# Kernel optimization log

Measured on AMD Instinct MI355X. Metric: run time of the kernel, lower is better.

The kernel has to match this reference:

```python
import jax, jax.numpy as jnp
import numpy as np
from jax import lax

DIM = 256
HEADS = 8
EPS = 1e-12  # torch F.normalize default eps
DN = ('NCHW', 'OIHW', 'NCHW')


def conv1x1(x, w):
    return lax.conv_general_dilated(x, w, (1, 1), 'VALID', dimension_numbers=DN)


def dwconv3x3(x, w):
    c = x.shape[1]
    return lax.conv_general_dilated(x, w, (1, 1), ((1, 1), (1, 1)),
                                    dimension_numbers=DN, feature_group_count=c)


def setup_inputs() -> dict:
    key = jax.random.key(0)
    ks = jax.random.split(key, 8)
    B, C, H, W = 4, DIM, 160, 160
    s = lambda fan: 1.0 / np.sqrt(fan)
    return {
        'low': jax.random.normal(ks[0], (B, C, H, W), jnp.float32),
        'high': jax.random.normal(ks[1], (B, C, H, W), jnp.float32),
        'q_w': jax.random.normal(ks[2], (C, C, 1, 1), jnp.float32) * s(C),
        'q_dw_w': jax.random.normal(ks[3], (C, 1, 3, 3), jnp.float32) * s(9),
        'kv_w': jax.random.normal(ks[4], (2 * C, C, 1, 1), jnp.float32) * s(C),
        'kv_dw_w': jax.random.normal(ks[5], (2 * C, 1, 3, 3), jnp.float32) * s(9),
        'proj_w': jax.random.normal(ks[6], (C, C, 1, 1), jnp.float32) * s(C),
        'temperature': jnp.ones((HEADS, 1, 1), jnp.float32),
    }


def reference(low, high, q_w, q_dw_w, kv_w, kv_dw_w, proj_w, temperature):
    B, C, H, W = low.shape
    hw = H * W
    ch = C // HEADS  # channels per head

    q = dwconv3x3(conv1x1(high, q_w), q_dw_w)           # [B, C, H, W]
    kv = dwconv3x3(conv1x1(low, kv_w), kv_dw_w)         # [B, 2C, H, W]
    k, v = jnp.split(kv, 2, axis=1)

    def heads(x):
        return x.reshape(B, HEADS, ch, hw)              # b head c (h w)

    q, k, v = heads(q), heads(k), heads(v)

    # L2-normalize along spatial dim (torch F.normalize semantics)
    q = q / jnp.maximum(jnp.linalg.norm(q, axis=-1, keepdims=True), EPS)
    k = k / jnp.maximum(jnp.linalg.norm(k, axis=-1, keepdims=True), EPS)

    attn = jnp.einsum('bhcn,bhdn->bhcd', q, k) * temperature  # [B, H, ch, ch]
    attn = jax.nn.softmax(attn, axis=-1)
    out = jnp.einsum('bhcd,bhdn->bhcn', attn, v)               # [B, H, ch, hw]

    out = out.reshape(B, C, H, W)
    return conv1x1(out, proj_w)
```

## Files before the change

### kernel.cpp

```cpp
#include <hip/hip_runtime.h>
#include <math.h>

#define HW 25600
#define IMGW 160
#define CDIM 256
#define NB 4
#define NHEADS 8
#define SZB ((long)CDIM * HW)

typedef __attribute__((ext_vector_type(8))) short short8v;
typedef __attribute__((ext_vector_type(4))) float f32x4;
typedef __attribute__((ext_vector_type(8))) unsigned short us8;

union FragU {
    us8 o;
    short8v s;
};

__device__ inline unsigned short f2bf(float f) {
    unsigned u = __float_as_uint(f);
    return (unsigned short)((u + 0x7fffu + ((u >> 16) & 1u)) >> 16);
}
__device__ inline float bf2f(unsigned short h) {
    return __uint_as_float(((unsigned)h) << 16);
}

__global__ __launch_bounds__(256) void cvtw_k(
    const float* __restrict__ w, unsigned short* __restrict__ o,
    int co_off, int nco)
{
    int idx = blockIdx.x * 256 + threadIdx.x;
    if (idx >= nco * 32) return;
    int g2 = idx & 3;
    int kt = (idx >> 2) & 7;
    int co = idx >> 5;
    const float* src = w + (long)(co_off + co) * CDIM + kt * 32 + g2 * 8;
    us8 v;
#pragma unroll
    for (int u = 0; u < 8; ++u) v[u] = f2bf(src[u]);
    int slot = g2 ^ ((co >> 1) & 3);
    *(us8*)(o + ((long)kt * nco + co) * 32 + slot * 8) = v;
}

__global__ __launch_bounds__(256) void cvtT2_k(
    const float* __restrict__ x, unsigned short* __restrict__ xs)
{
    __shared__ float tile[64][65];
    const int t = threadIdx.x;
    const int n0 = blockIdx.x * 64;
    const int c0 = blockIdx.y * 64;
    const long b = blockIdx.z;
    const float* xb = x + b * SZB;
    unsigned short* xo = xs + b * SZB;
#pragma unroll
    for (int it = 0; it < 4; ++it) {
        int row = (t >> 4) + it * 16;
        int col = (t & 15) * 4;
        float4 v = *(const float4*)(xb + (long)(c0 + row) * HW + n0 + col);
        tile[row][col]     = v.x; tile[row][col + 1] = v.y;
        tile[row][col + 2] = v.z; tile[row][col + 3] = v.w;
    }
    __syncthreads();
#pragma unroll
    for (int jt = 0; jt < 2; ++jt) {
        int nl = (t >> 3) + jt * 32;
        int cl = (t & 7) * 8;
        us8 o;
#pragma unroll
        for (int u = 0; u < 8; ++u) o[u] = f2bf(tile[cl + u][nl]);
        int n  = n0 + nl;
        int c  = c0 + cl;
        int kt = c >> 5;
        int g2 = (c >> 3) & 3;
        int slot = g2 ^ ((n >> 1) & 3);
        *(us8*)(xo + ((long)kt * HW + n) * 32 + slot * 8) = o;
    }
}

template<int OUTF32>
__global__ __launch_bounds__(256) void gemm2_k(
    const unsigned short* __restrict__ XS, const unsigned short* __restrict__ WS,
    void* __restrict__ outp, long xbs, long wbs, long obs, int nco)
{
    __shared__ __align__(16) unsigned short Wl[128 * 32];
    __shared__ __align__(16) unsigned short Xl[128 * 32];
    const int t  = threadIdx.x;
    const int l  = t & 63;
    const int wv = t >> 6;
    const int g  = l >> 4;
    const int ln = l & 15;
    const int n0  = blockIdx.x * 128;
    const int co0 = blockIdx.y * 128;
    const long b  = blockIdx.z;
    const unsigned short* Xb = XS + b * xbs;
    const unsigned short* Wb = WS + b * wbs;
    const int wr = wv >> 1, wc = wv & 1;

    f32x4 acc[4][4];
#pragma unroll
    for (int i = 0; i < 4; ++i)
#pragma unroll
        for (int j = 0; j < 4; ++j) acc[i][j] = (f32x4){0.f, 0.f, 0.f, 0.f};

    const int lrow = l >> 2;
    const int lgrp = l & 3;

    for (int kt = 0; kt < 8; ++kt) {
        __syncthreads();
#pragma unroll
        for (int ii = 0; ii < 2; ++ii) {
            int instr = wv * 2 + ii;
            int row = instr * 16 + lrow;
            const unsigned short* wsrc =
                Wb + ((long)kt * nco + co0 + row) * 32 + lgrp * 8;
            __builtin_amdgcn_global_load_lds(
                (const __attribute__((address_space(1))) void*)wsrc,
                (__attribute__((address_space(3))) void*)&Wl[instr * 512], 16, 0, 0);
            const unsigned short* xsrc =
                Xb + ((long)kt * HW + n0 + row) * 32 + lgrp * 8;
            __builtin_amdgcn_global_load_lds(
                (const __attribute__((address_space(1))) void*)xsrc,
                (__attribute__((address_space(3))) void*)&Xl[instr * 512], 16, 0, 0);
        }
        __syncthreads();

        FragU A_[4], B_[4];
#pragma unroll
        for (int i = 0; i < 4; ++i) {
            int row = wr * 64 + i * 16 + ln;
            int slot = g ^ ((row >> 1) & 3);
            A_[i].o = *(const us8*)&Wl[row * 32 + slot * 8];
        }
#pragma unroll
        for (int j = 0; j < 4; ++j) {
            int row = wc * 64 + j * 16 + ln;
            int slot = g ^ ((row >> 1) & 3);
            B_[j].o = *(const us8*)&Xl[row * 32 + slot * 8];
        }
#pragma unroll
        for (int i = 0; i < 4; ++i)
#pragma unroll
            for (int j = 0; j < 4; ++j)
                acc[i][j] = __builtin_amdgcn_mfma_f32_16x16x32_bf16(
                    A_[i].s, B_[j].s, acc[i][j], 0, 0, 0);
    }

    if (OUTF32) {
        float* ob = (float*)outp + b * obs;
#pragma unroll
        for (int i = 0; i < 4; ++i)
#pragma unroll
            for (int j = 0; j < 4; ++j) {
                long ocol = n0 + wc * 64 + j * 16 + ln;
#pragma unroll
                for (int r = 0; r < 4; ++r) {
                    long orow = co0 + wr * 64 + i * 16 + g * 4 + r;
                    ob[orow * HW + ocol] = acc[i][j][r];
                }
            }
    } else {
        unsigned short* ob = (unsigned short*)outp + b * obs;
#pragma unroll
        for (int i = 0; i < 4; ++i)
#pragma unroll
            for (int j = 0; j < 4; ++j) {
                long ocol = n0 + wc * 64 + j * 16 + ln;
#pragma unroll
                for (int r = 0; r < 4; ++r) {
                    long orow = co0 + wr * 64 + i * 16 + g * 4 + r;
                    ob[orow * HW + ocol] = f2bf(acc[i][j][r]);
                }
            }
    }
}

__global__ __launch_bounds__(256) void dwK_k(
    const unsigned short* __restrict__ A, const float* __restrict__ w,
    unsigned short* __restrict__ out)
{
    __shared__ unsigned short xsh[8][10][168];
    const int t = threadIdx.x;
    const int y0 = blockIdx.x * 8;
    const int c0 = blockIdx.y * 8;
    const long b = blockIdx.z;
    const unsigned short* Ab = A + b * SZB;

    for (int idx = t; idx < 1600; idx += 256) {
        int seg = idx % 20;
        int row = (idx / 20) % 10;
        int ch  = idx / 200;
        int yy  = y0 + row - 1;
        us8 v = (us8){0, 0, 0, 0, 0, 0, 0, 0};
        if (yy >= 0 && yy < IMGW)
            v = *(const us8*)(Ab + (long)(c0 + ch) * HW + yy * IMGW + seg * 8);
        *(us8*)&xsh[ch][row][seg * 8] = v;
    }
    __syncthreads();

    const int ch = t >> 5;
    const int rem = t & 31;
    const int ro = rem >> 2;
    const int xq = rem & 3;
    float wreg[9];
#pragma unroll
    for (int u = 0; u < 9; ++u) wreg[u] = w[(c0 + ch) * 9 + u];
    unsigned short* ob = out + b * SZB + (long)(c0 + ch) * HW + (y0 + ro) * IMGW;

#pragma unroll
    for (int xs = 0; xs < 5; ++xs) {
        int x = xq * 8 + xs * 32;
        float s[8];
#pragma unroll
        for (int p = 0; p < 8; ++p) s[p] = 0.f;
#pragma unroll
        for (int dy = 0; dy < 3; ++dy) {
            const unsigned short* rp = &xsh[ch][ro + dy][0];
            float r[10];
            r[0] = (x > 0) ? bf2f(rp[x - 1]) : 0.f;
            us8 mid = *(const us8*)&rp[x];
#pragma unroll
            for (int u = 0; u < 8; ++u) r[1 + u] = bf2f(mid[u]);
            r[9] = (x + 8 < IMGW) ? bf2f(rp[x + 8]) : 0.f;
            float w0 = wreg[dy * 3], w1 = wreg[dy * 3 + 1], w2 = wreg[dy * 3 + 2];
#pragma unroll
            for (int p = 0; p < 8; ++p)
                s[p] = fmaf(w0, r[p], fmaf(w1, r[p + 1], fmaf(w2, r[p + 2], s[p])));
        }
        us8 o;
#pragma unroll
        for (int p = 0; p < 8; ++p) o[p] = f2bf(s[p]);
        *(us8*)(ob + x) = o;
    }
}

__global__ __launch_bounds__(256) void dwV_k(
    const unsigned short* __restrict__ A, const float* __restrict__ w,
    unsigned short* __restrict__ out)
{
    __shared__ unsigned short xsh[16][6][168];
    __shared__ unsigned short osh[640][17];
    const int t = threadIdx.x;
    const int y0 = blockIdx.x * 4;
    const int c0 = blockIdx.y * 16;
    const long b = blockIdx.z;
    const unsigned short* Ab = A + b * SZB;

    for (int idx = t; idx < 1920; idx += 256) {
        int seg = idx % 20;
        int row = (idx / 20) % 6;
        int ch  = idx / 120;
        int yy  = y0 + row - 1;
        us8 v = (us8){0, 0, 0, 0, 0, 0, 0, 0};
        if (yy >= 0 && yy < IMGW)
            v = *(const us8*)(Ab + (long)(c0 + ch) * HW + yy * IMGW + seg * 8);
        *(us8*)&xsh[ch][row][seg * 8] = v;
    }
    __syncthreads();

    {
        const int ch = t >> 4;
        const int rem = t & 15;
        const int ro = rem >> 2;
        const int xq = rem & 3;
        float wreg[9];
#pragma unroll
        for (int u = 0; u < 9; ++u) wreg[u] = w[(c0 + ch) * 9 + u];
#pragma unroll
        for (int xs = 0; xs < 5; ++xs) {
            int x = xq * 8 + xs * 32;
            float s[8];
#pragma unroll
            for (int p = 0; p < 8; ++p) s[p] = 0.f;
#pragma unroll
            for (int dy = 0; dy < 3; ++dy) {
                const unsigned short* rp = &xsh[ch][ro + dy][0];
                float r[10];
                r[0] = (x > 0) ? bf2f(rp[x - 1]) : 0.f;
                us8 mid = *(const us8*)&rp[x];
#pragma unroll
                for (int u = 0; u < 8; ++u) r[1 + u] = bf2f(mid[u]);
                r[9] = (x + 8 < IMGW) ? bf2f(rp[x + 8]) : 0.f;
                float w0 = wreg[dy * 3], w1 = wreg[dy * 3 + 1], w2 = wreg[dy * 3 + 2];
#pragma unroll
                for (int p = 0; p < 8; ++p)
                    s[p] = fmaf(w0, r[p], fmaf(w1, r[p + 1], fmaf(w2, r[p + 2], s[p])));
            }
            int nl = ro * IMGW + x;
#pragma unroll
            for (int p = 0; p < 8; ++p) osh[nl + p][ch] = f2bf(s[p]);
        }
    }
    __syncthreads();

    for (int idx = t; idx < 1280; idx += 256) {
        int nl = idx >> 1;
        int c8 = (idx & 1) * 8;
        us8 o;
#pragma unroll
        for (int u = 0; u < 8; ++u) o[u] = osh[nl][c8 + u];
        int n  = y0 * IMGW + nl;
        int cg = c0 + c8;
        int kt = cg >> 5;
        int g2 = (cg >> 3) & 3;
        int slot = g2 ^ ((n >> 1) & 3);
        *(us8*)(out + b * SZB + ((long)kt * HW + n) * 32 + slot * 8) = o;
    }
}

__global__ __launch_bounds__(256) void gram_k(
    const unsigned short* __restrict__ q, const unsigned short* __restrict__ k,
    float* __restrict__ part_qk, float* __restrict__ part_sq_q,
    float* __restrict__ part_sq_k)
{
    __shared__ float Sred[4 * 1024];
    __shared__ float sqq_l[4][32];
    __shared__ float sqk_l[4][32];
    const int t  = threadIdx.x;
    const int l  = t & 63;
    const int wv = t >> 6;
    const int g  = l >> 4;
    const int ln = l & 15;
    const int chunk = blockIdx.x;
    const int h = blockIdx.y;
    const int b = blockIdx.z;

    f32x4 accS[2][2], accQ[2], accK[2];
#pragma unroll
    for (int i = 0; i < 2; ++i) {
        accQ[i] = (f32x4){0, 0, 0, 0};
        accK[i] = (f32x4){0, 0, 0, 0};
#pragma unroll
        for (int j = 0; j < 2; ++j) accS[i][j] = (f32x4){0, 0, 0, 0};
    }

    const unsigned short* qb = q + (long)b * SZB + (long)(h * 32) * HW;
    const unsigned short* kb = k + (long)b * SZB + (long)(h * 32) * HW;
    long nb = (long)chunk * 3200 + wv * 800;
    for (int s = 0; s < 25; ++s, nb += 32) {
        FragU aq[2], bk[2];
#pragma unroll
        for (int i = 0; i < 2; ++i)
            aq[i].o = *(const us8*)(qb + (long)(i * 16 + ln) * HW + nb + g * 8);
#pragma unroll
        for (int j = 0; j < 2; ++j)
            bk[j].o = *(const us8*)(kb + (long)(j * 16 + ln) * HW + nb + g * 8);
#pragma unroll
        for (int i = 0; i < 2; ++i)
#pragma unroll
            for (int j = 0; j < 2; ++j)
                accS[i][j] = __builtin_amdgcn_mfma_f32_16x16x32_bf16(
                    aq[i].s, bk[j].s, accS[i][j], 0, 0, 0);
#pragma unroll
        for (int i = 0; i < 2; ++i) {
            accQ[i] = __builtin_amdgcn_mfma_f32_16x16x32_bf16(
                aq[i].s, aq[i].s, accQ[i], 0, 0, 0);
            accK[i] = __builtin_amdgcn_mfma_f32_16x16x32_bf16(
                bk[i].s, bk[i].s, accK[i], 0, 0, 0);
        }
    }
#pragma unroll
    for (int i = 0; i < 2; ++i)
#pragma unroll
        for (int j = 0; j < 2; ++j)
#pragma unroll
            for (int r = 0; r < 4; ++r) {
                int row = i * 16 + g * 4 + r;
                int col = j * 16 + ln;
                Sred[wv * 1024 + row * 32 + col] = accS[i][j][r];
            }
#pragma unroll
    for (int i = 0; i < 2; ++i)
#pragma unroll
        for (int r = 0; r < 4; ++r)
            if (ln == g * 4 + r) {
                sqq_l[wv][i * 16 + g * 4 + r] = accQ[i][r];
                sqk_l[wv][i * 16 + g * 4 + r] = accK[i][r];
            }
    __syncthreads();
    const long pb = ((long)(b * NHEADS + h) * 8 + chunk);
#pragma unroll
    for (int e0 = 0; e0 < 4; ++e0) {
        int e = e0 * 256 + t;
        float v = Sred[e] + Sred[1024 + e] + Sred[2048 + e] + Sred[3072 + e];
        part_qk[pb * 1024 + e] = v;
    }
    if (t < 32)
        part_sq_q[pb * 32 + t] = sqq_l[0][t] + sqq_l[1][t] + sqq_l[2][t] + sqq_l[3][t];
    else if (t < 64) {
        int j = t - 32;
        part_sq_k[pb * 32 + j] = sqk_l[0][j] + sqk_l[1][j] + sqk_l[2][j] + sqk_l[3][j];
    }
}

__global__ __launch_bounds__(256) void attn_weff_k(
    const float* __restrict__ part_qk, const float* __restrict__ part_sq_q,
    const float* __restrict__ part_sq_k, const float* __restrict__ proj_w,
    const float* __restrict__ temp, unsigned short* __restrict__ weff_s)
{
    __shared__ float at[32 * 33];
    __shared__ float nq[32], nk[32];
    int bh = blockIdx.x;
    int b = bh >> 3, h = bh & 7;
    int t = threadIdx.x;
    long pb0 = (long)bh * 8;
    float4 s = make_float4(0, 0, 0, 0);
    for (int c = 0; c < 8; ++c) {
        float4 v = *(const float4*)(part_qk + (pb0 + c) * 1024 + t * 4);
        s.x += v.x; s.y += v.y; s.z += v.z; s.w += v.w;
    }
    if (t < 32) {
        float a = 0;
        for (int c = 0; c < 8; ++c) a += part_sq_q[(pb0 + c) * 32 + t];
        nq[t] = fmaxf(sqrtf(a), 1e-12f);
    } else if (t < 64) {
        int j = t - 32;
        float a = 0;
        for (int c = 0; c < 8; ++c) a += part_sq_k[(pb0 + c) * 32 + j];
        nk[j] = fmaxf(sqrtf(a), 1e-12f);
    }
    __syncthreads();
    float tp = temp[h];
    int ci = t >> 3, cj0 = (t & 7) * 4;
    at[ci * 33 + cj0 + 0] = s.x / (nq[ci] * nk[cj0 + 0]) * tp;
    at[ci * 33 + cj0 + 1] = s.y / (nq[ci] * nk[cj0 + 1]) * tp;
    at[ci * 33 + cj0 + 2] = s.z / (nq[ci] * nk[cj0 + 2]) * tp;
    at[ci * 33 + cj0 + 3] = s.w / (nq[ci] * nk[cj0 + 3]) * tp;
    __syncthreads();
    if (t < 32) {
        float m = -1e30f;
        for (int j = 0; j < 32; ++j) m = fmaxf(m, at[t * 33 + j]);
        float ss = 0;
        for (int j = 0; j < 32; ++j) {
            float e = expf(at[t * 33 + j] - m);
            at[t * 33 + j] = e;
            ss += e;
        }
        float inv = 1.f / ss;
        for (int j = 0; j < 32; ++j) at[t * 33 + j] *= inv;
    }
    __syncthreads();
    int co = t;
    float pw[32];
#pragma unroll
    for (int i2 = 0; i2 < 32; ++i2) pw[i2] = proj_w[(long)co * CDIM + h * 32 + i2];
    unsigned short* wb = weff_s + (long)b * 65536 + (long)h * (256 * 32) + co * 32;
    int swz = (co >> 1) & 3;
    for (int j = 0; j < 32; ++j) {
        float a = 0;
#pragma unroll
        for (int i2 = 0; i2 < 32; ++i2) a = fmaf(pw[i2], at[i2 * 33 + j], a);
        wb[((j >> 3) ^ swz) * 8 + (j & 7)] = f2bf(a);
    }
}

extern "C" void kernel_launch(void* const* d_in, const int* in_sizes, int n_in,
                              void* d_out, int out_size, void* d_ws, size_t ws_size,
                              hipStream_t stream)
{
    const float* low    = (const float*)d_in[0];
    const float* high   = (const float*)d_in[1];
    const float* q_w    = (const float*)d_in[2];
    const float* q_dw   = (const float*)d_in[3];
    const float* kv_w   = (const float*)d_in[4];
    const float* kv_dw  = (const float*)d_in[5];
    const float* proj_w = (const float*)d_in[6];
    const float* temp   = (const float*)d_in[7];
    float* out = (float*)d_out;

    unsigned short* usws = (unsigned short*)d_ws;
    unsigned short* XS   = usws;
    unsigned short* Areg = XS + 4 * SZB;
    unsigned short* VT   = Areg + 4 * SZB;
    unsigned short* wk_s = VT + 4 * SZB;
    unsigned short* wv_s = wk_s + 65536;
    unsigned short* wq_s = wv_s + 65536;
    unsigned short* weff_s = wq_s + 65536;
    float* part_qk   = (float*)(weff_s + 4L * 65536);
    float* part_sq_q = part_qk + 32L * 8 * 1024;
    float* part_sq_k = part_sq_q + 32L * 8 * 32;
    float* endp      = part_sq_k + 32L * 8 * 32;
    if (ws_size < (size_t)((char*)endp - (char*)d_ws)) return;

    unsigned short* K_all = (unsigned short*)d_out;
    unsigned short* Q_all = K_all + 4 * SZB;

    dim3 blk(256);

    cvtw_k<<<dim3(32), blk, 0, stream>>>(kv_w, wk_s, 0, 256);
    cvtw_k<<<dim3(32), blk, 0, stream>>>(kv_w, wv_s, 256, 256);
    cvtw_k<<<dim3(32), blk, 0, stream>>>(q_w, wq_s, 0, 256);

    cvtT2_k<<<dim3(400, 4, NB), blk, 0, stream>>>(low, XS);
    gemm2_k<0><<<dim3(200, 2, NB), blk, 0, stream>>>(XS, wk_s, Areg,
                                                     SZB, 0, SZB, 256);
    dwK_k<<<dim3(20, 32, NB), blk, 0, stream>>>(Areg, kv_dw, K_all);
    gemm2_k<0><<<dim3(200, 2, NB), blk, 0, stream>>>(XS, wv_s, Areg,
                                                     SZB, 0, SZB, 256);
    dwV_k<<<dim3(40, 16, NB), blk, 0, stream>>>(Areg, kv_dw + 256 * 9, VT);

    cvtT2_k<<<dim3(400, 4, NB), blk, 0, stream>>>(high, XS);
    gemm2_k<0><<<dim3(200, 2, NB), blk, 0, stream>>>(XS, wq_s, Areg,
                                                     SZB, 0, SZB, 256);
    dwK_k<<<dim3(20, 32, NB), blk, 0, stream>>>(Areg, q_dw, Q_all);

    gram_k<<<dim3(8, NHEADS, NB), blk, 0, stream>>>(Q_all, K_all, part_qk,
                                                    part_sq_q, part_sq_k);
    attn_weff_k<<<dim3(32), blk, 0, stream>>>(
        part_qk, part_sq_q, part_sq_k, proj_w, temp, weff_s);

    gemm2_k<1><<<dim3(200, 2, NB), blk, 0, stream>>>(VT, weff_s, out,
                                                     SZB, 65536, SZB, 256);
}
```

Measured before the change: 314.1 us.

## Fuse fp32-to-bf16 input conversion into GEMM and merge K/V projection GEMMs

```diff
diff --git a/kernel.cpp b/kernel.cpp
--- a/kernel.cpp
+++ b/kernel.cpp
@@ -15,6 +15,7 @@
 union FragU {
     us8 o;
     short8v s;
+    unsigned u32[4];
 };
 
 __device__ inline unsigned short f2bf(float f) {
@@ -26,73 +27,44 @@
 }
 
 __global__ __launch_bounds__(256) void cvtw_k(
-    const float* __restrict__ w, unsigned short* __restrict__ o,
-    int co_off, int nco)
+    const float* __restrict__ kv_w, const float* __restrict__ q_w,
+    unsigned short* __restrict__ wkv_s, unsigned short* __restrict__ wq_s)
 {
     int idx = blockIdx.x * 256 + threadIdx.x;
-    if (idx >= nco * 32) return;
     int g2 = idx & 3;
     int kt = (idx >> 2) & 7;
     int co = idx >> 5;
-    const float* src = w + (long)(co_off + co) * CDIM + kt * 32 + g2 * 8;
+    const float* src;
+    unsigned short* dst;
+    int nco, co_l;
+    if (co < 512) { src = kv_w; dst = wkv_s; nco = 512; co_l = co; }
+    else          { src = q_w;  dst = wq_s;  nco = 256; co_l = co - 512; }
+    src += (long)co_l * CDIM + kt * 32 + g2 * 8;
     us8 v;
 #pragma unroll
     for (int u = 0; u < 8; ++u) v[u] = f2bf(src[u]);
-    int slot = g2 ^ ((co >> 1) & 3);
-    *(us8*)(o + ((long)kt * nco + co) * 32 + slot * 8) = v;
-}
-
-__global__ __launch_bounds__(256) void cvtT2_k(
-    const float* __restrict__ x, unsigned short* __restrict__ xs)
-{
-    __shared__ float tile[64][65];
-    const int t = threadIdx.x;
-    const int n0 = blockIdx.x * 64;
-    const int c0 = blockIdx.y * 64;
-    const long b = blockIdx.z;
-    const float* xb = x + b * SZB;
-    unsigned short* xo = xs + b * SZB;
-#pragma unroll
-    for (int it = 0; it < 4; ++it) {
-        int row = (t >> 4) + it * 16;
-        int col = (t & 15) * 4;
-        float4 v = *(const float4*)(xb + (long)(c0 + row) * HW + n0 + col);
-        tile[row][col]     = v.x; tile[row][col + 1] = v.y;
-        tile[row][col + 2] = v.z; tile[row][col + 3] = v.w;
-    }
-    __syncthreads();
-#pragma unroll
-    for (int jt = 0; jt < 2; ++jt) {
-        int nl = (t >> 3) + jt * 32;
-        int cl = (t & 7) * 8;
-        us8 o;
-#pragma unroll
-        for (int u = 0; u < 8; ++u) o[u] = f2bf(tile[cl + u][nl]);
-        int n  = n0 + nl;
-        int c  = c0 + cl;
-        int kt = c >> 5;
-        int g2 = (c >> 3) & 3;
-        int slot = g2 ^ ((n >> 1) & 3);
-        *(us8*)(xo + ((long)kt * HW + n) * 32 + slot * 8) = o;
-    }
-}
-
-template<int OUTF32>
+    int slot = g2 ^ ((co_l >> 1) & 3);
+    *(us8*)(dst + ((long)kt * nco + co_l) * 32 + slot * 8) = v;
+}
+
+template<int OUTF32, int XF32>
 __global__ __launch_bounds__(256) void gemm2_k(
-    const unsigned short* __restrict__ XS, const unsigned short* __restrict__ WS,
+    const void* __restrict__ Xv, const unsigned short* __restrict__ WS,
     void* __restrict__ outp, long xbs, long wbs, long obs, int nco)
 {
     __shared__ __align__(16) unsigned short Wl[128 * 32];
-    __shared__ __align__(16) unsigned short Xl[128 * 32];
+    __shared__ __align__(16) char XBuf[XF32 ? (32 * 132 * 4) : (128 * 32 * 2)];
+    float* Xf = (float*)XBuf;
+    unsigned short* Xl = (unsigned short*)XBuf;
+
     const int t  = threadIdx.x;
     const int l  = t & 63;
     const int wv = t >> 6;
     const int g  = l >> 4;
     const int ln = l & 15;
-    const int n0  = blockIdx.x * 128;
-    const int co0 = blockIdx.y * 128;
+    const int co0 = blockIdx.x * 128;
+    const int n0  = blockIdx.y * 128;
     const long b  = blockIdx.z;
-    const unsigned short* Xb = XS + b * xbs;
     const unsigned short* Wb = WS + b * wbs;
     const int wr = wv >> 1, wc = wv & 1;
 
@@ -116,11 +88,30 @@
             __builtin_amdgcn_global_load_lds(
                 (const __attribute__((address_space(1))) void*)wsrc,
                 (__attribute__((address_space(3))) void*)&Wl[instr * 512], 16, 0, 0);
-            const unsigned short* xsrc =
-                Xb + ((long)kt * HW + n0 + row) * 32 + lgrp * 8;
-            __builtin_amdgcn_global_load_lds(
-                (const __attribute__((address_space(1))) void*)xsrc,
-                (__attribute__((address_space(3))) void*)&Xl[instr * 512], 16, 0, 0);
+        }
+        if (XF32) {
+            const float* Xb = (const float*)Xv + b * xbs;
+#pragma unroll
+            for (int r = 0; r < 4; ++r) {
+                int idx = r * 256 + t;
+                int row = idx >> 5;
+                int c4  = idx & 31;
+                float4 v = *(const float4*)(Xb + (long)(kt * 32 + row) * HW
+                                            + n0 + c4 * 4);
+                *(float4*)&Xf[row * 132 + c4 * 4] = v;
+            }
+        } else {
+            const unsigned short* Xb = (const unsigned short*)Xv + b * xbs;
+#pragma unroll
+            for (int ii = 0; ii < 2; ++ii) {
+                int instr = wv * 2 + ii;
+                int row = instr * 16 + lrow;
+                const unsigned short* xsrc =
+                    Xb + ((long)kt * HW + n0 + row) * 32 + lgrp * 8;
+                __builtin_amdgcn_global_load_lds(
+                    (const __attribute__((address_space(1))) void*)xsrc,
+                    (__attribute__((address_space(3))) void*)&Xl[instr * 512], 16, 0, 0);
+            }
         }
         __syncthreads();
 
@@ -131,11 +122,27 @@
             int slot = g ^ ((row >> 1) & 3);
             A_[i].o = *(const us8*)&Wl[row * 32 + slot * 8];
         }
-#pragma unroll
-        for (int j = 0; j < 4; ++j) {
-            int row = wc * 64 + j * 16 + ln;
-            int slot = g ^ ((row >> 1) & 3);
-            B_[j].o = *(const us8*)&Xl[row * 32 + slot * 8];
+        if (XF32) {
+#pragma unroll
+            for (int j = 0; j < 4; ++j) {
+                int n = wc * 64 + j * 16 + ln;
+#pragma unroll
+                for (int e2 = 0; e2 < 4; ++e2) {
+                    float lo = Xf[(g * 8 + e2 * 2) * 132 + n];
+                    float hi = Xf[(g * 8 + e2 * 2 + 1) * 132 + n];
+                    unsigned r;
+                    asm("v_cvt_pk_bf16_f32 %0, %1, %2"
+                        : "=v"(r) : "v"(lo), "v"(hi));
+                    B_[j].u32[e2] = r;
+                }
+            }
+        } else {
+#pragma unroll
+            for (int j = 0; j < 4; ++j) {
+                int row = wc * 64 + j * 16 + ln;
+                int slot = g ^ ((row >> 1) & 3);
+                B_[j].o = *(const us8*)&Xl[row * 32 + slot * 8];
+            }
         }
 #pragma unroll
         for (int i = 0; i < 4; ++i)
@@ -176,14 +183,14 @@
 
 __global__ __launch_bounds__(256) void dwK_k(
     const unsigned short* __restrict__ A, const float* __restrict__ w,
-    unsigned short* __restrict__ out)
+    unsigned short* __restrict__ out, long bstride)
 {
     __shared__ unsigned short xsh[8][10][168];
     const int t = threadIdx.x;
     const int y0 = blockIdx.x * 8;
     const int c0 = blockIdx.y * 8;
     const long b = blockIdx.z;
-    const unsigned short* Ab = A + b * SZB;
+    const unsigned short* Ab = A + b * bstride;
 
     for (int idx = t; idx < 1600; idx += 256) {
         int seg = idx % 20;
@@ -235,7 +242,7 @@
 
 __global__ __launch_bounds__(256) void dwV_k(
     const unsigned short* __restrict__ A, const float* __restrict__ w,
-    unsigned short* __restrict__ out)
+    unsigned short* __restrict__ out, long bstride)
 {
     __shared__ unsigned short xsh[16][6][168];
     __shared__ unsigned short osh[640][17];
@@ -243,7 +250,7 @@
     const int y0 = blockIdx.x * 4;
     const int c0 = blockIdx.y * 16;
     const long b = blockIdx.z;
-    const unsigned short* Ab = A + b * SZB;
+    const unsigned short* Ab = A + b * bstride;
 
     for (int idx = t; idx < 1920; idx += 256) {
         int seg = idx % 20;
@@ -468,12 +475,10 @@
     float* out = (float*)d_out;
 
     unsigned short* usws = (unsigned short*)d_ws;
-    unsigned short* XS   = usws;
-    unsigned short* Areg = XS + 4 * SZB;
-    unsigned short* VT   = Areg + 4 * SZB;
-    unsigned short* wk_s = VT + 4 * SZB;
-    unsigned short* wv_s = wk_s + 65536;
-    unsigned short* wq_s = wv_s + 65536;
+    unsigned short* Areg = usws;
+    unsigned short* VT   = Areg + 8 * SZB;
+    unsigned short* wkv_s = VT + 4 * SZB;
+    unsigned short* wq_s  = wkv_s + 131072;
     unsigned short* weff_s = wq_s + 65536;
     float* part_qk   = (float*)(weff_s + 4L * 65536);
     float* part_sq_q = part_qk + 32L * 8 * 1024;
@@ -486,28 +491,23 @@
 
     dim3 blk(256);
 
-    cvtw_k<<<dim3(32), blk, 0, stream>>>(kv_w, wk_s, 0, 256);
-    cvtw_k<<<dim3(32), blk, 0, stream>>>(kv_w, wv_s, 256, 256);
-    cvtw_k<<<dim3(32), blk, 0, stream>>>(q_w, wq_s, 0, 256);
-
-    cvtT2_k<<<dim3(400, 4, NB), blk, 0, stream>>>(low, XS);
-    gemm2_k<0><<<dim3(200, 2, NB), blk, 0, stream>>>(XS, wk_s, Areg,
-                                                     SZB, 0, SZB, 256);
-    dwK_k<<<dim3(20, 32, NB), blk, 0, stream>>>(Areg, kv_dw, K_all);
-    gemm2_k<0><<<dim3(200, 2, NB), blk, 0, stream>>>(XS, wv_s, Areg,
-                                                     SZB, 0, SZB, 256);
-    dwV_k<<<dim3(40, 16, NB), blk, 0, stream>>>(Areg, kv_dw + 256 * 9, VT);
-
-    cvtT2_k<<<dim3(400, 4, NB), blk, 0, stream>>>(high, XS);
-    gemm2_k<0><<<dim3(200, 2, NB), blk, 0, stream>>>(XS, wq_s, Areg,
-                                                     SZB, 0, SZB, 256);
-    dwK_k<<<dim3(20, 32, NB), blk, 0, stream>>>(Areg, q_dw, Q_all);
+    cvtw_k<<<dim3(96), blk, 0, stream>>>(kv_w, q_w, wkv_s, wq_s);
+
+    gemm2_k<0, 1><<<dim3(4, 200, NB), blk, 0, stream>>>(
+        low, wkv_s, Areg, SZB, 0, 2 * SZB, 512);
+    dwK_k<<<dim3(20, 32, NB), blk, 0, stream>>>(Areg, kv_dw, K_all, 2 * SZB);
+    dwV_k<<<dim3(40, 16, NB), blk, 0, stream>>>(Areg + 256L * HW,
+                                                kv_dw + 256 * 9, VT, 2 * SZB);
+
+    gemm2_k<0, 1><<<dim3(2, 200, NB), blk, 0, stream>>>(
+        high, wq_s, Areg, SZB, 0, 2 * SZB, 256);
+    dwK_k<<<dim3(20, 32, NB), blk, 0, stream>>>(Areg, q_dw, Q_all, 2 * SZB);
 
     gram_k<<<dim3(8, NHEADS, NB), blk, 0, stream>>>(Q_all, K_all, part_qk,
                                                     part_sq_q, part_sq_k);
     attn_weff_k<<<dim3(32), blk, 0, stream>>>(
         part_qk, part_sq_q, part_sq_k, proj_w, temp, weff_s);
 
-    gemm2_k<1><<<dim3(200, 2, NB), blk, 0, stream>>>(VT, weff_s, out,
-                                                     SZB, 65536, SZB, 256);
-}
+    gemm2_k<1, 0><<<dim3(2, 200, NB), blk, 0, stream>>>(VT, weff_s, out,
+                                                        SZB, 65536, SZB, 256);
+}
```

Measured after the change: 318.9 us. About the same (+1.5%).
